# Kernel tuning notes

Measured on AMD Instinct MI355X. Metric: run time of the kernel, lower is better.

## Reference

```python
import jax, jax.numpy as jnp
import numpy as np

TOP_K = 2
EPS = 1e-9


def setup_inputs() -> dict:
    key = jax.random.key(0)
    ks = jax.random.split(key, 5)
    B, S, D, H, E, G = 4, 2048, 1024, 1024, 8, 256
    x = jax.random.normal(ks[0], (B, S, D), dtype=jnp.float32)
    # gate MLP (top_k_gating with hidden_size=gating_size)
    Wg1 = jax.random.normal(ks[1], (D, G), dtype=jnp.float32) * (1.0 / np.sqrt(D))
    Wg2 = jax.random.normal(ks[2], (G, E), dtype=jnp.float32) * (1.0 / np.sqrt(G))
    # experts: uniform(-1/D, 1/D) as in init_experts
    W_in = jax.random.uniform(ks[3], (E, D, H), dtype=jnp.float32, minval=-1.0 / D, maxval=1.0 / D)
    W_out = jax.random.uniform(ks[4], (E, H, D), dtype=jnp.float32, minval=-1.0 / D, maxval=1.0 / D)
    return {"x": x, "Wg1": Wg1, "Wg2": Wg2, "W_in": W_in, "W_out": W_out}


def _gate(xf, Wg1, Wg2):
    # gate MLP -> softmax probs over experts
    h = jnp.tanh(xf @ Wg1)                      # [N, G]
    probs = jax.nn.softmax(h @ Wg2, axis=-1)    # [N, E]
    top_v, top_i = jax.lax.top_k(probs, TOP_K)  # [N, k]
    N, E = probs.shape
    # dense gate matrix: zeros except top-k entries (== compute_gating combine weights)
    gates = jnp.zeros((N, E), probs.dtype).at[jnp.arange(N)[:, None], top_i].set(top_v)
    return gates, probs


def _mi_loss(probs):
    # mutual-information aux loss: minimize -(H(mean_p) - mean H(p))
    p_mean = probs.mean(axis=0)
    h_mean = -jnp.sum(p_mean * jnp.log(p_mean + EPS))
    mean_h = -jnp.mean(jnp.sum(probs * jnp.log(probs + EPS), axis=-1))
    return -h_mean + mean_h


def reference(x, Wg1, Wg2, W_in, W_out):
    B, S, D = x.shape
    xf = x.reshape(-1, D)                        # [N, D]
    gates, probs = _gate(xf, Wg1, Wg2)           # [N, E]
    # per-expert FFN: relu(x @ W_in[e]) @ W_out[e], combined with top-k gates.
    h = jnp.einsum('nd,edh->enh', xf, W_in)      # [E, N, H]
    h = jax.nn.relu(h)
    y = jnp.einsum('enh,ehd->end', h, W_out)     # [E, N, D]
    out = jnp.einsum('ne,end->nd', gates, y)     # gate-weighted combine
    loss = _mi_loss(probs)
    return out.reshape(B, S, D), loss
```

## Files before the change

kernel.cpp:

```cpp
#include <hip/hip_runtime.h>


#define N_TOK 8192
#define DIM   1024
#define HID   1024
#define NEXP  8
#define GDIM  256
#define NPAIR (N_TOK * 2)
#define HB_ROWS (NPAIR + 256)
#define MT2   72
#define GAP_P 2e-3f
#define SPLIT_SCALE 2048.0f
#define NPREP (4096 + 64 + 4096)

typedef __attribute__((ext_vector_type(4))) float    f32x4;
typedef __attribute__((ext_vector_type(8))) _Float16 f16x8;

static __device__ __forceinline__ void async_ld16(const void* g, void* l) {
  __builtin_amdgcn_global_load_lds(
      (const __attribute__((address_space(1))) unsigned int*)g,
      (__attribute__((address_space(3))) unsigned int*)l, 16, 0, 0);
}

__global__ __launch_bounds__(256) void prep_kernel(const float* __restrict__ x,
                                                   _Float16* __restrict__ xh,
                                                   const float* __restrict__ Wg1,
                                                   _Float16* __restrict__ WhT,
                                                   _Float16* __restrict__ WlT,
                                                   const float* __restrict__ Win,
                                                   const float* __restrict__ Wout,
                                                   _Float16* __restrict__ WinT,
                                                   _Float16* __restrict__ WoutT,
                                                   int* __restrict__ hdr) {
  __shared__ float t[64][65];
  int bx = blockIdx.x;
  int tid = threadIdx.x;
  if (bx < 4096) {
    size_t o = ((size_t)bx * 256 + tid) * 8;
    float4 v0 = *(const float4*)(x + o);
    float4 v1 = *(const float4*)(x + o + 4);
    float v[8] = {v0.x, v0.y, v0.z, v0.w, v1.x, v1.y, v1.z, v1.w};
    f16x8 h;
#pragma unroll
    for (int k = 0; k < 8; ++k) h[k] = (_Float16)v[k];
    *(f16x8*)(xh + o) = h;
  } else if (bx < 4096 + 64) {
    int b = bx - 4096;
    int k0 = (b & 15) * 64, g0 = (b >> 4) * 64;
    int col4 = tid & 15, ib = tid >> 4;
#pragma unroll
    for (int q = 0; q < 4; ++q) {
      int i = ib * 4 + q;
      *(float4*)&t[i][col4 * 4] = *(const float4*)&Wg1[(size_t)(k0 + i) * GDIM + g0 + col4 * 4];
    }
    __syncthreads();
#pragma unroll
    for (int q = 0; q < 2; ++q) {
      int c = tid * 2 + q;
      int j = c >> 3, i8 = (c & 7) * 8;
      f16x8 h, l;
#pragma unroll
      for (int k = 0; k < 8; ++k) {
        float v = t[i8 + k][j];
        _Float16 hi = (_Float16)v;
        h[k] = hi;
        l[k] = (_Float16)((v - (float)hi) * SPLIT_SCALE);
      }
      *(f16x8*)&WhT[(size_t)(g0 + j) * DIM + k0 + i8] = h;
      *(f16x8*)&WlT[(size_t)(g0 + j) * DIM + k0 + i8] = l;
    }
  } else if (bx < NPREP) {
    int b = bx - 4160;
    int z = b >> 8, rem = b & 255;
    const float* src = (z < NEXP ? Win : Wout) + (size_t)(z & 7) * DIM * HID;
    _Float16*    dst = (z < NEXP ? WinT : WoutT) + (size_t)(z & 7) * DIM * HID;
    int i0 = (rem & 15) * 64, j0 = (rem >> 4) * 64;
    int col4 = tid & 15, ib = tid >> 4;
#pragma unroll
    for (int q = 0; q < 4; ++q) {
      int i = ib * 4 + q;
      *(float4*)&t[i][col4 * 4] = *(const float4*)&src[(size_t)(i0 + i) * 1024 + j0 + col4 * 4];
    }
    __syncthreads();
#pragma unroll
    for (int q = 0; q < 2; ++q) {
      int c = tid * 2 + q;
      int j = c >> 3, i8 = (c & 7) * 8;
      f16x8 h;
#pragma unroll
      for (int k = 0; k < 8; ++k) h[k] = (_Float16)t[i8 + k][j];
      *(f16x8*)&dst[(size_t)(j0 + j) * 1024 + i0 + i8] = h;
    }
  } else {
    hdr[tid * 2 + 0] = 0;
    hdr[tid * 2 + 1] = 0;
  }
}

__global__ __launch_bounds__(256) void gemm_gate_kernel(const _Float16* __restrict__ xh,
                                                        const _Float16* __restrict__ WhT,
                                                        const _Float16* __restrict__ WlT,
                                                        const float* __restrict__ Wg2,
                                                        int* __restrict__ top_i,
                                                        float* __restrict__ top_v,
                                                        float* __restrict__ lossacc,
                                                        int* __restrict__ counts,
                                                        int* __restrict__ nflag,
                                                        int* __restrict__ flaglist) {
  __shared__ __align__(16) _Float16 Ah[32 * 32];
  __shared__ __align__(16) _Float16 Bh[256 * 32];
  __shared__ __align__(16) _Float16 Bl[256 * 32];
  __shared__ float hsm[32][260];
  __shared__ float psum[8];
  __shared__ float entsum;
  __shared__ int cnts[8];
  int m0 = blockIdx.x * 32;
  int tid = threadIdx.x, lane = tid & 63, wave = tid >> 6;
  int wr = (wave >> 1) * 16;
  int wc = (wave & 1) * 128;
  if (tid < 8) { psum[tid] = 0.f; cnts[tid] = 0; }
  if (tid == 0) entsum = 0.f;

  int srcslot = ((lane & 3) ^ ((lane >> 4) & 3)) << 3;
  size_t asrc = (size_t)(m0 + wave * 16 + (lane >> 2)) * DIM + srcslot;
  size_t bsrc[4];
#pragma unroll
  for (int p = 0; p < 4; ++p)
    bsrc[p] = (size_t)(wave * 16 + p * 64 + (lane >> 2)) * DIM + srcslot;
  int rdoff = ((lane >> 4) ^ ((lane >> 2) & 3)) << 3;
  f32x4 acc[8] = {}, accl[8] = {};

  for (int k0 = 0; k0 < DIM; k0 += 32) {
    __syncthreads();
    if (wave < 2) async_ld16(xh + asrc + k0, Ah + wave * 512);
#pragma unroll
    for (int p = 0; p < 4; ++p) {
      async_ld16(WhT + bsrc[p] + k0, Bh + wave * 512 + p * 2048);
      async_ld16(WlT + bsrc[p] + k0, Bl + wave * 512 + p * 2048);
    }
    __syncthreads();
    f16x8 a = *(const f16x8*)&Ah[(wr + (lane & 15)) * 32 + rdoff];
#pragma unroll
    for (int n = 0; n < 8; ++n) {
      f16x8 bh = *(const f16x8*)&Bh[(wc + n * 16 + (lane & 15)) * 32 + rdoff];
      f16x8 bl = *(const f16x8*)&Bl[(wc + n * 16 + (lane & 15)) * 32 + rdoff];
      acc[n]  = __builtin_amdgcn_mfma_f32_16x16x32_f16(a, bh, acc[n], 0, 0, 0);
      accl[n] = __builtin_amdgcn_mfma_f32_16x16x32_f16(a, bl, accl[n], 0, 0, 0);
    }
  }
#pragma unroll
  for (int n = 0; n < 8; ++n) {
#pragma unroll
    for (int i = 0; i < 4; ++i) {
      int row = wr + ((lane >> 4) << 2) + i;
      int col = wc + n * 16 + (lane & 15);
      hsm[row][col] = tanhf(acc[n][i] + accl[n][i] * (1.0f / SPLIT_SCALE));
    }
  }
  __syncthreads();

  int tok = tid >> 3, sl = tid & 7;
  float lg[8] = {0, 0, 0, 0, 0, 0, 0, 0};
#pragma unroll
  for (int j = 0; j < 32; ++j) {
    int g = sl + j * 8;
    float hv = hsm[tok][g];
#pragma unroll
    for (int e = 0; e < 8; ++e) lg[e] = fmaf(hv, Wg2[g * 8 + e], lg[e]);
  }
#pragma unroll
  for (int e = 0; e < 8; ++e) {
    lg[e] += __shfl_xor(lg[e], 4);
    lg[e] += __shfl_xor(lg[e], 2);
    lg[e] += __shfl_xor(lg[e], 1);
  }
  if (sl == 0) {
    int token = m0 + tok;
    float mx = lg[0];
#pragma unroll
    for (int e = 1; e < 8; ++e) mx = fmaxf(mx, lg[e]);
    float p[8], s = 0.f;
#pragma unroll
    for (int e = 0; e < 8; ++e) { p[e] = expf(lg[e] - mx); s += p[e]; }
    float inv = 1.f / s, ent = 0.f;
    int i0 = 0, i1 = 0;
    float v0 = -1.f, v1 = -1.f, v2 = -1.f;
#pragma unroll
    for (int e = 0; e < 8; ++e) {
      p[e] *= inv;
      ent += p[e] * logf(p[e] + 1e-9f);
      if (p[e] > v0)      { v2 = v1; v1 = v0; i1 = i0; v0 = p[e]; i0 = e; }
      else if (p[e] > v1) { v2 = v1; v1 = p[e]; i1 = e; }
      else if (p[e] > v2) { v2 = p[e]; }
    }
    top_i[token * 2 + 0] = i0; top_i[token * 2 + 1] = i1;
    top_v[token * 2 + 0] = v0; top_v[token * 2 + 1] = v1;
    if (v1 - v2 < GAP_P) {
      int ix = atomicAdd(nflag, 1);
      if (ix < 8192) flaglist[ix] = token;
    }
#pragma unroll
    for (int e = 0; e < 8; ++e) atomicAdd(&psum[e], p[e]);
    atomicAdd(&entsum, ent);
    atomicAdd(&cnts[i0], 1);
    atomicAdd(&cnts[i1], 1);
  }
  __syncthreads();
  if (tid < 8) { atomicAdd(&lossacc[tid], psum[tid]); atomicAdd(&counts[tid], cnts[tid]); }
  if (tid == 8) atomicAdd(&lossacc[8], entsum);
}

__global__ __launch_bounds__(256) void regate_kernel(const float* __restrict__ x,
                                                     const float* __restrict__ Wg1,
                                                     const float* __restrict__ Wg2,
                                                     const int* __restrict__ nflag,
                                                     const int* __restrict__ flaglist,
                                                     int* __restrict__ top_i,
                                                     float* __restrict__ top_v,
                                                     int* __restrict__ counts) {
  __shared__ float xs[DIM];
  __shared__ float wsum[4][8];
  int tid = threadIdx.x;
  int nf = *nflag; if (nf > 8192) nf = 8192;
  for (int it = blockIdx.x; it < nf; it += gridDim.x) {
    int token = flaglist[it];
    const float* xr = x + (size_t)token * DIM;
    *(float4*)&xs[tid * 4] = *(const float4*)&xr[tid * 4];
    __syncthreads();
    float s0 = 0.f, s1 = 0.f, s2 = 0.f, s3 = 0.f;
    float s4 = 0.f, s5 = 0.f, s6 = 0.f, s7 = 0.f;
    for (int k = 0; k < DIM; k += 8) {
      s0 = fmaf(xs[k + 0], Wg1[(size_t)(k + 0) * GDIM + tid], s0);
      s1 = fmaf(xs[k + 1], Wg1[(size_t)(k + 1) * GDIM + tid], s1);
      s2 = fmaf(xs[k + 2], Wg1[(size_t)(k + 2) * GDIM + tid], s2);
      s3 = fmaf(xs[k + 3], Wg1[(size_t)(k + 3) * GDIM + tid], s3);
      s4 = fmaf(xs[k + 4], Wg1[(size_t)(k + 4) * GDIM + tid], s4);
      s5 = fmaf(xs[k + 5], Wg1[(size_t)(k + 5) * GDIM + tid], s5);
      s6 = fmaf(xs[k + 6], Wg1[(size_t)(k + 6) * GDIM + tid], s6);
      s7 = fmaf(xs[k + 7], Wg1[(size_t)(k + 7) * GDIM + tid], s7);
    }
    float hgv = tanhf(((s0 + s1) + (s2 + s3)) + ((s4 + s5) + (s6 + s7)));
    float lg[8];
#pragma unroll
    for (int e = 0; e < 8; ++e) lg[e] = hgv * Wg2[tid * 8 + e];
#pragma unroll
    for (int e = 0; e < 8; ++e) {
      lg[e] += __shfl_xor(lg[e], 32);
      lg[e] += __shfl_xor(lg[e], 16);
      lg[e] += __shfl_xor(lg[e], 8);
      lg[e] += __shfl_xor(lg[e], 4);
      lg[e] += __shfl_xor(lg[e], 2);
      lg[e] += __shfl_xor(lg[e], 1);
    }
    int wv = tid >> 6;
    if ((tid & 63) == 0) {
#pragma unroll
      for (int e = 0; e < 8; ++e) wsum[wv][e] = lg[e];
    }
    __syncthreads();
    if (tid == 0) {
      float l[8];
#pragma unroll
      for (int e = 0; e < 8; ++e)
        l[e] = (wsum[0][e] + wsum[1][e]) + (wsum[2][e] + wsum[3][e]);
      float mx = l[0];
#pragma unroll
      for (int e = 1; e < 8; ++e) mx = fmaxf(mx, l[e]);
      float p[8], s = 0.f;
#pragma unroll
      for (int e = 0; e < 8; ++e) { p[e] = expf(l[e] - mx); s += p[e]; }
      float inv = 1.f / s;
      int i0 = 0, i1 = 0;
      float v0 = -1.f, v1 = -1.f;
#pragma unroll
      for (int e = 0; e < 8; ++e) {
        p[e] *= inv;
        if (p[e] > v0)      { v1 = v0; i1 = i0; v0 = p[e]; i0 = e; }
        else if (p[e] > v1) { v1 = p[e]; i1 = e; }
      }
      int oi0 = top_i[token * 2 + 0], oi1 = top_i[token * 2 + 1];
      if (oi0 != i0 || oi1 != i1) {
        atomicSub(&counts[oi0], 1); atomicSub(&counts[oi1], 1);
        atomicAdd(&counts[i0], 1);  atomicAdd(&counts[i1], 1);
      }
      top_i[token * 2 + 0] = i0; top_i[token * 2 + 1] = i1;
      top_v[token * 2 + 0] = v0; top_v[token * 2 + 1] = v1;
    }
    __syncthreads();
  }
}

__global__ __launch_bounds__(256) void fill_kernel(const int* __restrict__ top_i,
                                                   const float* __restrict__ top_v,
                                                   const int* __restrict__ counts,
                                                   int* __restrict__ cursors,
                                                   int* __restrict__ ptok,
                                                   float* __restrict__ pgate,
                                                   int* __restrict__ rowof) {
  __shared__ int lcnt[8];
  __shared__ int lbase[8];
  __shared__ int soff[8];
  int tid = threadIdx.x;
  int n = blockIdx.x * 256 + tid;
  if (tid == 0) {
    int a = 0;
#pragma unroll
    for (int e = 0; e < 8; ++e) { soff[e] = a; a += counts[e]; }
  }
  if (tid < 8) lcnt[tid] = 0;
  __syncthreads();
  int e0 = top_i[n * 2 + 0], e1 = top_i[n * 2 + 1];
  int p0 = atomicAdd(&lcnt[e0], 1);
  int p1 = atomicAdd(&lcnt[e1], 1);
  __syncthreads();
  if (tid < 8) lbase[tid] = atomicAdd(&cursors[tid], lcnt[tid]);
  __syncthreads();
  int r0 = soff[e0] + lbase[e0] + p0;
  int r1 = soff[e1] + lbase[e1] + p1;
  ptok[r0] = n;  pgate[r0] = top_v[n * 2 + 0];  rowof[n * 2 + 0] = r0;
  ptok[r1] = n;  pgate[r1] = top_v[n * 2 + 1];  rowof[n * 2 + 1] = r1;
}

#define GEMM_PIPE(STAGE_EXPR)                                                        \
  STAGE_EXPR(0, 0);                                                                  \
  STAGE_EXPR(32, 1);                                                                 \
  asm volatile("s_waitcnt vmcnt(3)" ::: "memory");                                   \
  __builtin_amdgcn_s_barrier();                                                      \
  int cbuf = 0;                                                                      \
  for (int t = 0; t < 32; ++t) {                                                     \
    f16x8 a[4], b[4];                                                                \
    _Pragma("unroll")                                                                \
    for (int m = 0; m < 4; ++m)                                                      \
      a[m] = *(const f16x8*)&Als[cbuf][(wr + m * 16 + (lane & 15)) * 32 + rdoff];    \
    _Pragma("unroll")                                                                \
    for (int n = 0; n < 4; ++n)                                                      \
      b[n] = *(const f16x8*)&Bls[cbuf][(wc + n * 16 + (lane & 15)) * 32 + rdoff];    \
    asm volatile("s_waitcnt lgkmcnt(0)" ::: "memory");                               \
    __builtin_amdgcn_sched_barrier(0);                                               \
    __builtin_amdgcn_s_barrier();                                                    \
    bool st = (t + 2 < 32);                                                          \
    if (st) { STAGE_EXPR((t + 2) * 32, cbuf); }                                      \
    __builtin_amdgcn_s_setprio(1);                                                   \
    _Pragma("unroll")                                                                \
    for (int m = 0; m < 4; ++m)                                                      \
      _Pragma("unroll")                                                              \
      for (int n = 0; n < 4; ++n)                                                    \
        acc[m][n] = __builtin_amdgcn_mfma_f32_16x16x32_f16(a[m], b[n], acc[m][n], 0, 0, 0); \
    __builtin_amdgcn_s_setprio(0);                                                   \
    if (st) asm volatile("s_waitcnt vmcnt(3)" ::: "memory");                         \
    else    asm volatile("s_waitcnt vmcnt(0)" ::: "memory");                         \
    __builtin_amdgcn_sched_barrier(0);                                               \
    __builtin_amdgcn_s_barrier();                                                    \
    cbuf ^= 1;                                                                       \
  }

__global__ __launch_bounds__(512) void gemm1_kernel(const _Float16* __restrict__ xh,
                                                    const _Float16* __restrict__ WinT,
                                                    _Float16* __restrict__ hb,
                                                    const int* __restrict__ counts,
                                                    const int* __restrict__ ptok) {
  __shared__ __align__(16) _Float16 Als[2][256 * 32];
  __shared__ __align__(16) _Float16 Bls[2][128 * 32];
  int bx = blockIdx.x;
  int loc = (bx & 7) * 9 + (bx >> 3);
  int base = 0, cnt = 0, e;
  for (e = 0; e < NEXP; ++e) {
    cnt = counts[e];
    int mts = (cnt + 255) >> 8;
    if (loc < mts) break;
    loc -= mts; base += cnt;
  }
  if (e == NEXP) return;
  int row0 = base + (loc << 8);
  int rmax = cnt - (loc << 8);
  int n0 = blockIdx.y << 7;
  int tid = threadIdx.x, wave = tid >> 6, lane = tid & 63;
  int wr = (wave >> 1) << 6, wc = (wave & 1) << 6;

  const _Float16* WB = WinT + (size_t)e * DIM * HID;
  int scol = (((lane & 3) ^ (lane >> 4)) << 3);
  size_t asrc[2];
#pragma unroll
  for (int j = 0; j < 2; ++j) {
    int r = wave * 32 + j * 16 + (lane >> 2);
    int tok = ptok[(r < rmax) ? (row0 + r) : base];
    asrc[j] = (size_t)tok * DIM + scol;
  }
  int brow = tid >> 2;
  size_t bsrc = (size_t)(n0 + brow) * DIM + (((tid & 3) ^ ((tid >> 4) & 3)) << 3);
  int aldst = wave * 1024;
  int bldst = wave * 512;
  int rdoff = ((lane >> 4) ^ ((lane >> 2) & 3)) << 3;
  f32x4 acc[4][4] = {};

#define STAGE1(K0, CB)                                          \
  do {                                                          \
    async_ld16(xh + asrc[0] + (K0), &Als[(CB)][aldst]);         \
    async_ld16(xh + asrc[1] + (K0), &Als[(CB)][aldst + 512]);   \
    async_ld16(WB + bsrc + (K0), &Bls[(CB)][bldst]);            \
  } while (0)

  GEMM_PIPE(STAGE1)
#undef STAGE1

#pragma unroll
  for (int m = 0; m < 4; ++m) {
#pragma unroll
    for (int i = 0; i < 4; ++i) {
      int r = wr + m * 16 + ((lane >> 4) << 2) + i;
      if (r < rmax) {
        _Float16* hrow = hb + (size_t)(row0 + r) * HID;
#pragma unroll
        for (int n = 0; n < 4; ++n)
          hrow[n0 + wc + n * 16 + (lane & 15)] = (_Float16)fmaxf(acc[m][n][i], 0.f);
      }
    }
  }
}

__global__ __launch_bounds__(512) void gemm2_kernel(const _Float16* __restrict__ hb,
                                                    const _Float16* __restrict__ WoutT,
                                                    _Float16* __restrict__ yb,
                                                    const int* __restrict__ counts,
                                                    const float* __restrict__ pgate) {
  __shared__ __align__(16) _Float16 Als[2][256 * 32];
  __shared__ __align__(16) _Float16 Bls[2][128 * 32];
  int bx = blockIdx.x;
  int loc = (bx & 7) * 9 + (bx >> 3);
  int base = 0, cnt = 0, e;
  for (e = 0; e < NEXP; ++e) {
    cnt = counts[e];
    int mts = (cnt + 255) >> 8;
    if (loc < mts) break;
    loc -= mts; base += cnt;
  }
  if (e == NEXP) return;
  int row0 = base + (loc << 8);
  int rmax = cnt - (loc << 8);
  int n0 = blockIdx.y << 7;
  int tid = threadIdx.x, wave = tid >> 6, lane = tid & 63;
  int wr = (wave >> 1) << 6, wc = (wave & 1) << 6;

  const _Float16* WB = WoutT + (size_t)e * DIM * HID;
  int scol = (((lane & 3) ^ (lane >> 4)) << 3);
  size_t asrc[2];
#pragma unroll
  for (int j = 0; j < 2; ++j) {
    int r = wave * 32 + j * 16 + (lane >> 2);
    asrc[j] = (size_t)(row0 + r) * HID + scol;
  }
  int brow = tid >> 2;
  size_t bsrc = (size_t)(n0 + brow) * DIM + (((tid & 3) ^ ((tid >> 4) & 3)) << 3);
  int aldst = wave * 1024;
  int bldst = wave * 512;
  int rdoff = ((lane >> 4) ^ ((lane >> 2) & 3)) << 3;
  f32x4 acc[4][4] = {};

#define STAGE2(K0, CB)                                          \
  do {                                                          \
    async_ld16(hb + asrc[0] + (K0), &Als[(CB)][aldst]);         \
    async_ld16(hb + asrc[1] + (K0), &Als[(CB)][aldst + 512]);   \
    async_ld16(WB + bsrc + (K0), &Bls[(CB)][bldst]);            \
  } while (0)

  GEMM_PIPE(STAGE2)
#undef STAGE2

#pragma unroll
  for (int m = 0; m < 4; ++m) {
#pragma unroll
    for (int i = 0; i < 4; ++i) {
      int r = wr + m * 16 + ((lane >> 4) << 2) + i;
      if (r < rmax) {
        int gr = row0 + r;
        float gv = pgate[gr];
        _Float16* yrow = yb + (size_t)gr * DIM;
#pragma unroll
        for (int n = 0; n < 4; ++n)
          yrow[n0 + wc + n * 16 + (lane & 15)] = (_Float16)(gv * acc[m][n][i]);
      }
    }
  }
}

__global__ __launch_bounds__(256) void combine_kernel(const _Float16* __restrict__ yb,
                                                      const int* __restrict__ rowof,
                                                      float* __restrict__ out,
                                                      const float* __restrict__ lossacc,
                                                      float* __restrict__ lossdst) {
  int tid = threadIdx.x;
  int token = blockIdx.x * 2 + (tid >> 7);
  int d0 = (tid & 127) * 8;
  int r0 = rowof[token * 2 + 0];
  int r1 = rowof[token * 2 + 1];
  f16x8 a = *(const f16x8*)&yb[(size_t)r0 * DIM + d0];
  f16x8 b = *(const f16x8*)&yb[(size_t)r1 * DIM + d0];
  float* orow = out + (size_t)token * DIM + d0;
  float4 o0, o1;
  o0.x = (float)a[0] + (float)b[0]; o0.y = (float)a[1] + (float)b[1];
  o0.z = (float)a[2] + (float)b[2]; o0.w = (float)a[3] + (float)b[3];
  o1.x = (float)a[4] + (float)b[4]; o1.y = (float)a[5] + (float)b[5];
  o1.z = (float)a[6] + (float)b[6]; o1.w = (float)a[7] + (float)b[7];
  *(float4*)orow = o0;
  *(float4*)(orow + 4) = o1;
  if (blockIdx.x == 0 && tid == 0) {
    float t1 = 0.f;
#pragma unroll
    for (int e = 0; e < 8; ++e) {
      float pm = lossacc[e] * (1.f / (float)N_TOK);
      t1 += pm * logf(pm + 1e-9f);
    }
    lossdst[0] = t1 - lossacc[8] * (1.f / (float)N_TOK);
  }
}

extern "C" void kernel_launch(void* const* d_in, const int* in_sizes, int n_in,
                              void* d_out, int out_size, void* d_ws, size_t ws_size,
                              hipStream_t stream) {
  const float* x    = (const float*)d_in[0];
  const float* Wg1  = (const float*)d_in[1];
  const float* Wg2  = (const float*)d_in[2];
  const float* Win  = (const float*)d_in[3];
  const float* Wout = (const float*)d_in[4];
  float* out = (float*)d_out;

  char* ws = (char*)d_ws;
  size_t off = 0;
  auto alloc = [&](size_t bytes) -> void* {
    void* p = ws + off;
    off = (off + bytes + 255) & ~(size_t)255;
    return p;
  };
  int*   counts  = (int*)alloc(32);
  int*   cursors = (int*)alloc(32);
  float* lossacc = (float*)alloc(64);
  int*   nflag   = (int*)alloc(32);
  int*   flaglist= (int*)alloc(8192 * 4);
  int*   top_i   = (int*)alloc((size_t)NPAIR * 4);
  float* top_v   = (float*)alloc((size_t)NPAIR * 4);
  int*   ptok    = (int*)alloc((size_t)NPAIR * 4);
  float* pgate   = (float*)alloc((size_t)NPAIR * 4);
  int*   rowof   = (int*)alloc((size_t)NPAIR * 4);
  char*  scratch1 = (char*)alloc((size_t)HB_ROWS * HID * 2);
  _Float16* Wg1hT  = (_Float16*)scratch1;
  _Float16* Wg1lsT = Wg1hT + (size_t)GDIM * DIM;
  _Float16* hb     = (_Float16*)scratch1;
  _Float16* xh    = (_Float16*)alloc((size_t)N_TOK * DIM * 2);
  _Float16* WinT  = (_Float16*)alloc((size_t)NEXP * DIM * HID * 2);
  _Float16* WoutT = (_Float16*)alloc((size_t)NEXP * DIM * HID * 2);
  _Float16* yb = xh;
  (void)ws_size; (void)in_sizes; (void)n_in;

  prep_kernel<<<NPREP + 1, 256, 0, stream>>>(x, xh, Wg1, Wg1hT, Wg1lsT,
                                             Win, Wout, WinT, WoutT, (int*)d_ws);
  gemm_gate_kernel<<<N_TOK / 32, 256, 0, stream>>>(xh, Wg1hT, Wg1lsT, Wg2, top_i, top_v,
                                                   lossacc, counts, nflag, flaglist);
  regate_kernel<<<256, 256, 0, stream>>>(x, Wg1, Wg2, nflag, flaglist, top_i, top_v, counts);
  fill_kernel<<<N_TOK / 256, 256, 0, stream>>>(top_i, top_v, counts, cursors,
                                               ptok, pgate, rowof);
  gemm1_kernel<<<dim3(MT2, HID / 128), 512, 0, stream>>>(xh, WinT, hb, counts, ptok);
  gemm2_kernel<<<dim3(MT2, DIM / 128), 512, 0, stream>>>(hb, WoutT, yb, counts, pgate);
  combine_kernel<<<N_TOK / 2, 256, 0, stream>>>(yb, rowof, out, lossacc,
                                                out + (size_t)N_TOK * DIM);
}
```

Measured before the change: 255.7 us.

## Overlap expert weight fp16 transpose with gating GEMM in one launch

The transposing cast of the expert weights W_in and W_out to fp16 moves out of the prep kernel into extra blocks of the gating GEMM kernel. The gate blocks and the weight-cast blocks now run concurrently, which should let the bandwidth-bound cast hide behind the gate GEMM compute. Shared memory is now one union buffer sized for the larger gate layout. That large allocation may limit how many of the many cast blocks fit on each CU at once.

```diff
diff --git a/kernel.cpp b/kernel.cpp
--- a/kernel.cpp
+++ b/kernel.cpp
@@ -11,7 +11,7 @@
 #define MT2   72
 #define GAP_P 2e-3f
 #define SPLIT_SCALE 2048.0f
-#define NPREP (4096 + 64 + 4096)
+#define NPREP1 (4096 + 64 + 1)
 
 typedef __attribute__((ext_vector_type(4))) float    f32x4;
 typedef __attribute__((ext_vector_type(8))) _Float16 f16x8;
@@ -22,16 +22,12 @@
       (__attribute__((address_space(3))) unsigned int*)l, 16, 0, 0);
 }
 
-__global__ __launch_bounds__(256) void prep_kernel(const float* __restrict__ x,
-                                                   _Float16* __restrict__ xh,
-                                                   const float* __restrict__ Wg1,
-                                                   _Float16* __restrict__ WhT,
-                                                   _Float16* __restrict__ WlT,
-                                                   const float* __restrict__ Win,
-                                                   const float* __restrict__ Wout,
-                                                   _Float16* __restrict__ WinT,
-                                                   _Float16* __restrict__ WoutT,
-                                                   int* __restrict__ hdr) {
+__global__ __launch_bounds__(256) void prep1_kernel(const float* __restrict__ x,
+                                                    _Float16* __restrict__ xh,
+                                                    const float* __restrict__ Wg1,
+                                                    _Float16* __restrict__ WhT,
+                                                    _Float16* __restrict__ WlT,
+                                                    int* __restrict__ hdr) {
   __shared__ float t[64][65];
   int bx = blockIdx.x;
   int tid = threadIdx.x;
@@ -69,35 +65,13 @@
       *(f16x8*)&WhT[(size_t)(g0 + j) * DIM + k0 + i8] = h;
       *(f16x8*)&WlT[(size_t)(g0 + j) * DIM + k0 + i8] = l;
     }
-  } else if (bx < NPREP) {
-    int b = bx - 4160;
-    int z = b >> 8, rem = b & 255;
-    const float* src = (z < NEXP ? Win : Wout) + (size_t)(z & 7) * DIM * HID;
-    _Float16*    dst = (z < NEXP ? WinT : WoutT) + (size_t)(z & 7) * DIM * HID;
-    int i0 = (rem & 15) * 64, j0 = (rem >> 4) * 64;
-    int col4 = tid & 15, ib = tid >> 4;
-#pragma unroll
-    for (int q = 0; q < 4; ++q) {
-      int i = ib * 4 + q;
-      *(float4*)&t[i][col4 * 4] = *(const float4*)&src[(size_t)(i0 + i) * 1024 + j0 + col4 * 4];
-    }
-    __syncthreads();
-#pragma unroll
-    for (int q = 0; q < 2; ++q) {
-      int c = tid * 2 + q;
-      int j = c >> 3, i8 = (c & 7) * 8;
-      f16x8 h;
-#pragma unroll
-      for (int k = 0; k < 8; ++k) h[k] = (_Float16)t[i8 + k][j];
-      *(f16x8*)&dst[(size_t)(j0 + j) * 1024 + i0 + i8] = h;
-    }
   } else {
     hdr[tid * 2 + 0] = 0;
     hdr[tid * 2 + 1] = 0;
   }
 }
 
-__global__ __launch_bounds__(256) void gemm_gate_kernel(const _Float16* __restrict__ xh,
+__global__ __launch_bounds__(256) void gate_cast_kernel(const _Float16* __restrict__ xh,
                                                         const _Float16* __restrict__ WhT,
                                                         const _Float16* __restrict__ WlT,
                                                         const float* __restrict__ Wg2,
@@ -106,16 +80,50 @@
                                                         float* __restrict__ lossacc,
                                                         int* __restrict__ counts,
                                                         int* __restrict__ nflag,
-                                                        int* __restrict__ flaglist) {
-  __shared__ __align__(16) _Float16 Ah[32 * 32];
-  __shared__ __align__(16) _Float16 Bh[256 * 32];
-  __shared__ __align__(16) _Float16 Bl[256 * 32];
-  __shared__ float hsm[32][260];
+                                                        int* __restrict__ flaglist,
+                                                        const float* __restrict__ Win,
+                                                        const float* __restrict__ Wout,
+                                                        _Float16* __restrict__ WinT,
+                                                        _Float16* __restrict__ WoutT) {
+  __shared__ __align__(16) char smem[68096];
+  int bx = blockIdx.x;
+  int tid = threadIdx.x;
+
+  if (bx >= 256) {
+    float (*t)[65] = (float(*)[65])smem;
+    int b = bx - 256;
+    int z = b >> 8, rem = b & 255;
+    const float* src = (z < NEXP ? Win : Wout) + (size_t)(z & 7) * DIM * HID;
+    _Float16*    dst = (z < NEXP ? WinT : WoutT) + (size_t)(z & 7) * DIM * HID;
+    int i0 = (rem & 15) * 64, j0 = (rem >> 4) * 64;
+    int col4 = tid & 15, ib = tid >> 4;
+#pragma unroll
+    for (int q = 0; q < 4; ++q) {
+      int i = ib * 4 + q;
+      *(float4*)&t[i][col4 * 4] = *(const float4*)&src[(size_t)(i0 + i) * 1024 + j0 + col4 * 4];
+    }
+    __syncthreads();
+#pragma unroll
+    for (int q = 0; q < 2; ++q) {
+      int c = tid * 2 + q;
+      int j = c >> 3, i8 = (c & 7) * 8;
+      f16x8 h;
+#pragma unroll
+      for (int k = 0; k < 8; ++k) h[k] = (_Float16)t[i8 + k][j];
+      *(f16x8*)&dst[(size_t)(j0 + j) * 1024 + i0 + i8] = h;
+    }
+    return;
+  }
+
+  _Float16* Ah = (_Float16*)smem;
+  _Float16* Bh = (_Float16*)(smem + 2048);
+  _Float16* Bl = (_Float16*)(smem + 18432);
+  float (*hsm)[260] = (float(*)[260])(smem + 34816);
   __shared__ float psum[8];
   __shared__ float entsum;
   __shared__ int cnts[8];
-  int m0 = blockIdx.x * 32;
-  int tid = threadIdx.x, lane = tid & 63, wave = tid >> 6;
+  int m0 = bx * 32;
+  int lane = tid & 63, wave = tid >> 6;
   int wr = (wave >> 1) * 16;
   int wc = (wave & 1) * 128;
   if (tid < 8) { psum[tid] = 0.f; cnts[tid] = 0; }
@@ -551,10 +559,10 @@
   _Float16* yb = xh;
   (void)ws_size; (void)in_sizes; (void)n_in;
 
-  prep_kernel<<<NPREP + 1, 256, 0, stream>>>(x, xh, Wg1, Wg1hT, Wg1lsT,
-                                             Win, Wout, WinT, WoutT, (int*)d_ws);
-  gemm_gate_kernel<<<N_TOK / 32, 256, 0, stream>>>(xh, Wg1hT, Wg1lsT, Wg2, top_i, top_v,
-                                                   lossacc, counts, nflag, flaglist);
+  prep1_kernel<<<NPREP1, 256, 0, stream>>>(x, xh, Wg1, Wg1hT, Wg1lsT, (int*)d_ws);
+  gate_cast_kernel<<<256 + 4096, 256, 0, stream>>>(xh, Wg1hT, Wg1lsT, Wg2, top_i, top_v,
+                                                   lossacc, counts, nflag, flaglist,
+                                                   Win, Wout, WinT, WoutT);
   regate_kernel<<<256, 256, 0, stream>>>(x, Wg1, Wg2, nflag, flaglist, top_i, top_v, counts);
   fill_kernel<<<N_TOK / 256, 256, 0, stream>>>(top_i, top_v, counts, cursors,
                                                ptok, pgate, rowof);
```

Result: faster. 246.1 us (-3.8%).
